# Optimization experiments

Hardware: AMD Instinct MI355X
Metric: run time of the kernel (lower is better)

The kernel has to match this reference:

```python
import jax, jax.numpy as jnp
import numpy as np

EMBED_DIM = 768
NUM_HEADS = 12
HEAD_DIM = EMBED_DIM // NUM_HEADS
SCALE = HEAD_DIM ** -0.5
LN_EPS = 1e-5


def layer_norm(x, gamma, beta):
    mu = jnp.mean(x, axis=-1, keepdims=True)
    var = jnp.var(x, axis=-1, keepdims=True)
    return (x - mu) * jax.lax.rsqrt(var + LN_EPS) * gamma + beta


def setup_inputs() -> dict:
    key = jax.random.key(0)
    ks = jax.random.split(key, 10)
    B, N, M, C = 4, 4096, 256, EMBED_DIM
    inp = {
        "input_tokens": jax.random.normal(ks[0], (B, N, C), dtype=jnp.float32),
        "query_tokens": jax.random.normal(ks[1], (B, M, C), dtype=jnp.float32),
        "Wq": jax.random.normal(ks[2], (C, C), dtype=jnp.float32) * 0.02,
        "bq": jnp.zeros((C,), dtype=jnp.float32),
        "Wk": jax.random.normal(ks[3], (C, C), dtype=jnp.float32) * 0.02,
        "bk": jnp.zeros((C,), dtype=jnp.float32),
        "Wv": jax.random.normal(ks[4], (C, C), dtype=jnp.float32) * 0.02,
        "bv": jnp.zeros((C,), dtype=jnp.float32),
        "gq_ln": jnp.ones((C,), dtype=jnp.float32),
        "bq_ln": jnp.zeros((C,), dtype=jnp.float32),
        "gk_ln": jnp.ones((C,), dtype=jnp.float32),
        "bk_ln": jnp.zeros((C,), dtype=jnp.float32),
    }
    return inp


def reference(input_tokens, query_tokens, Wq, bq, Wk, bk, Wv, bv,
              gq_ln, bq_ln, gk_ln, bk_ln):
    B, N, C = input_tokens.shape
    _, M, _ = query_tokens.shape
    H, D = NUM_HEADS, HEAD_DIM

    # v: Linear only (no LayerNorm on the attn=None path)
    v = (input_tokens @ Wv.T + bv).reshape(B, N, H, D).transpose(0, 2, 1, 3)   # [B,H,N,D]
    # q, k: Linear -> LayerNorm over full embed_dim, then split heads
    q = layer_norm(query_tokens @ Wq.T + bq, gq_ln, bq_ln)
    q = q.reshape(B, M, H, D).transpose(0, 2, 1, 3) * SCALE                    # [B,H,M,D]
    k = layer_norm(input_tokens @ Wk.T + bk, gk_ln, bk_ln)
    k = k.reshape(B, N, H, D).transpose(0, 2, 1, 3)                            # [B,H,N,D]

    attn = jax.nn.softmax(jnp.einsum('bhmd,bhnd->bhmn', q, k), axis=-1)        # [B,H,M,N]
    out = jnp.einsum('bhmn,bhnd->bhmd', attn, v)                               # [B,H,M,D]
    out = out.transpose(0, 2, 1, 3).reshape(B, M, C)
    return (query_tokens + out, attn)
```

## Files before the change

### kernel.cpp

```cpp
#include <hip/hip_runtime.h>
#include <math.h>

#define BB 4
#define NN 4096
#define MM 256
#define CC 768
#define HH 12
#define DD 64
#define SCALEF 0.125f
#define LN_EPSF 1e-5f

typedef __attribute__((ext_vector_type(4))) float f32x4;
typedef __attribute__((ext_vector_type(16))) float f32x16;
typedef __attribute__((ext_vector_type(8))) _Float16 f16x8;
typedef __attribute__((ext_vector_type(4))) _Float16 f16x4;

__device__ __forceinline__ void gldh(const _Float16* g, _Float16* l) {
    __builtin_amdgcn_global_load_lds(
        (const __attribute__((address_space(1))) void*)g,
        (__attribute__((address_space(3))) void*)l, 16, 0, 0);
}

__global__ __launch_bounds__(256) void conv_f16(
    const float* __restrict__ x, _Float16* __restrict__ y, long long n)
{
    long long i = ((long long)blockIdx.x * 256 + threadIdx.x) * 8;
    const long long stride = (long long)gridDim.x * 256 * 8;
    for (; i < n; i += stride) {
        float4 a = *(const float4*)(x + i);
        float4 b = *(const float4*)(x + i + 4);
        f16x8 o;
        o[0] = (_Float16)a.x; o[1] = (_Float16)a.y;
        o[2] = (_Float16)a.z; o[3] = (_Float16)a.w;
        o[4] = (_Float16)b.x; o[5] = (_Float16)b.y;
        o[6] = (_Float16)b.z; o[7] = (_Float16)b.w;
        *(f16x8*)(y + i) = o;
    }
}

__global__ __launch_bounds__(256) void proj_kv_f16(
    const _Float16* __restrict__ Xh,
    const _Float16* __restrict__ X2h,
    const _Float16* __restrict__ Wkh, const _Float16* __restrict__ Wqh,
    const _Float16* __restrict__ Wvh,
    const float* __restrict__ bk, const float* __restrict__ bq,
    const float* __restrict__ bv,
    _Float16* __restrict__ Klin, _Float16* __restrict__ Qlin,
    _Float16* __restrict__ Vth)
{
    __shared__ _Float16 As[2][4096];
    __shared__ _Float16 Bks[2][4096];
    __shared__ _Float16 Bvs[2][4096];

    const int bid = blockIdx.x;
    const _Float16* Ag; const _Float16* Bkg;
    const float* biask; _Float16* outk;
    bool hasV;
    int bm, bn;
    if (bid < 768) {
        bm = bid & 127; bn = bid >> 7;
        Ag = Xh; Bkg = Wkh; biask = bk; outk = Klin; hasV = true;
    } else {
        const int sid = bid - 768;
        bm = sid & 7; bn = sid >> 3;
        Ag = X2h; Bkg = Wqh; biask = bq; outk = Qlin; hasV = false;
    }
    const int row0 = bm * 128, col0 = bn * 128;

    const int tid = threadIdx.x;
    const int w = tid >> 6, lane = tid & 63;
    const int wr = w >> 1, wc = w & 1;
    const int fr = lane & 15, kg = lane >> 4;

    f32x4 acck[4][4], accv[4][4];
#pragma unroll
    for (int m = 0; m < 4; ++m)
#pragma unroll
        for (int n = 0; n < 4; ++n) {
            acck[m][n] = (f32x4){0.f, 0.f, 0.f, 0.f};
            accv[m][n] = (f32x4){0.f, 0.f, 0.f, 0.f};
        }

#define STAGE(sel, kt)                                                           \
    do {                                                                         \
        const int kk = (kt) << 5;                                                \
        _Pragma("unroll")                                                        \
        for (int i = 0; i < 2; ++i) {                                            \
            const int cbase = (i * 4 + w) * 64;                                  \
            const int c = cbase + lane;                                          \
            const int row = c >> 2, ks = (c & 3) << 3;                           \
            gldh(Ag  + (size_t)(row0 + row) * CC + kk + ks, &As[sel][cbase * 8]);\
            gldh(Bkg + (size_t)(col0 + row) * CC + kk + ks, &Bks[sel][cbase * 8]);\
            gldh(Wvh + (size_t)(col0 + row) * CC + kk + ks, &Bvs[sel][cbase * 8]);\
        }                                                                        \
    } while (0)

    STAGE(0, 0);
    int cur = 0;
    const int nk = CC >> 5;
    for (int kt = 0; kt < nk; ++kt) {
        __syncthreads();
        if (kt + 1 < nk) STAGE(cur ^ 1, kt + 1);
        const _Float16* lA = As[cur];
        const _Float16* lBk = Bks[cur];
        const _Float16* lBv = Bvs[cur];
        f16x8 a[4];
#pragma unroll
        for (int m = 0; m < 4; ++m)
            a[m] = *(const f16x8*)(lA + (wr * 64 + m * 16 + fr) * 32 + kg * 8);
#pragma unroll
        for (int n = 0; n < 4; ++n) {
            f16x8 bkf = *(const f16x8*)(lBk + (wc * 64 + n * 16 + fr) * 32 + kg * 8);
            __builtin_amdgcn_s_setprio(1);
#pragma unroll
            for (int m = 0; m < 4; ++m)
                acck[m][n] = __builtin_amdgcn_mfma_f32_16x16x32_f16(
                    a[m], bkf, acck[m][n], 0, 0, 0);
            __builtin_amdgcn_s_setprio(0);
            f16x8 bvf = *(const f16x8*)(lBv + (wc * 64 + n * 16 + fr) * 32 + kg * 8);
            __builtin_amdgcn_s_setprio(1);
#pragma unroll
            for (int m = 0; m < 4; ++m)
                accv[m][n] = __builtin_amdgcn_mfma_f32_16x16x32_f16(
                    a[m], bvf, accv[m][n], 0, 0, 0);
            __builtin_amdgcn_s_setprio(0);
        }
        cur ^= 1;
    }
#undef STAGE

    {
        float bvv[4];
#pragma unroll
        for (int n = 0; n < 4; ++n)
            bvv[n] = biask[col0 + wc * 64 + n * 16 + fr];
#pragma unroll
        for (int m = 0; m < 4; ++m)
#pragma unroll
            for (int n = 0; n < 4; ++n) {
                const int col = col0 + wc * 64 + n * 16 + fr;
#pragma unroll
                for (int r = 0; r < 4; ++r) {
                    const int row = row0 + wr * 64 + m * 16 + kg * 4 + r;
                    outk[(size_t)row * CC + col] = (_Float16)(acck[m][n][r] + bvv[n]);
                }
            }
    }
    if (hasV) {
        const int b = row0 >> 12;
        const int rb = row0 & 4095;
#pragma unroll
        for (int n = 0; n < 4; ++n) {
            const int cg = col0 + wc * 64 + n * 16 + fr;
            const int hh = cg >> 6, d = cg & 63;
            const float bb = bv[cg];
            _Float16* vrow = Vth + ((size_t)((b * HH + hh) * DD + d)) * NN + rb + wr * 64;
#pragma unroll
            for (int m = 0; m < 4; ++m) {
                f16x4 v4;
#pragma unroll
                for (int r = 0; r < 4; ++r)
                    v4[r] = (_Float16)(accv[m][n][r] + bb);
                *(f16x4*)(vrow + m * 16 + kg * 4) = v4;
            }
        }
    }
}

__global__ __launch_bounds__(256) void ln_rows_f16(
    const _Float16* __restrict__ Y, _Float16* __restrict__ outh,
    const float* __restrict__ g, const float* __restrict__ be, const float scale)
{
    const int row = blockIdx.x;
    const _Float16* y = Y + (size_t)row * CC;
    const int tid = threadIdx.x;
    float x0 = (float)y[tid], x1 = (float)y[tid + 256], x2 = (float)y[tid + 512];
    float s = x0 + x1 + x2;
    float q = x0 * x0 + x1 * x1 + x2 * x2;
#pragma unroll
    for (int o = 32; o >= 1; o >>= 1) {
        s += __shfl_xor(s, o, 64);
        q += __shfl_xor(q, o, 64);
    }
    __shared__ float sh_s[4], sh_q[4];
    const int w = tid >> 6;
    if ((tid & 63) == 0) { sh_s[w] = s; sh_q[w] = q; }
    __syncthreads();
    s = sh_s[0] + sh_s[1] + sh_s[2] + sh_s[3];
    q = sh_q[0] + sh_q[1] + sh_q[2] + sh_q[3];
    const float mu  = s * (1.f / 768.f);
    const float var = q * (1.f / 768.f) - mu * mu;
    const float inv = rsqrtf(var + LN_EPSF);
    _Float16* o = outh + (size_t)row * CC;
    o[tid]       = (_Float16)(((x0 - mu) * inv * g[tid]       + be[tid])       * scale);
    o[tid + 256] = (_Float16)(((x1 - mu) * inv * g[tid + 256] + be[tid + 256]) * scale);
    o[tid + 512] = (_Float16)(((x2 - mu) * inv * g[tid + 512] + be[tid + 512]) * scale);
}

__global__ __launch_bounds__(256, 4) void attn_stats(
    const _Float16* __restrict__ Qh,
    const _Float16* __restrict__ Kh,
    float* __restrict__ stats)
{
    __shared__ __align__(16) unsigned char smem[37888];
    _Float16* Kl = (_Float16*)smem;
    _Float16* Ql = (_Float16*)(smem + 32768);
    float (*red)[32][2] = (float(*)[32][2])(smem + 36864);

    const int tid = threadIdx.x;
    const int w = tid >> 6, lane = tid & 63;
    const int l5 = lane >> 5, lm = lane & 31;
    const int bid = blockIdx.x;
    const int mt = bid / 192;
    const int rem = bid % 192;
    const int bh = rem >> 2, ns = rem & 3;
    const int h = bh % HH, b = bh / HH;
    const int qr0 = mt * 32;
    const int nb = ns * 1024;

#define STAGEK(sel, c0)                                                         \
    _Pragma("unroll")                                                           \
    for (int i = 0; i < 4; ++i) {                                               \
        const int L = i * 256 + tid;                                            \
        const int n = L >> 3, pos = L & 7;                                      \
        gldh(Kh + (size_t)(b * NN + (c0) + n) * CC + h * DD + ((pos ^ (n & 7)) << 3), \
             &Kl[(sel) * 8192 + (i * 256 + w * 64) * 8]);                       \
    }

    {
        const int n = tid >> 3, pos = tid & 7;
        gldh(Qh + (size_t)(b * MM + qr0 + n) * CC + h * DD + ((pos ^ (n & 7)) << 3),
             &Ql[(w * 64) * 8]);
    }
    STAGEK(0, nb);
    __syncthreads();
    f16x8 qf[4];
#pragma unroll
    for (int ks = 0; ks < 4; ++ks)
        qf[ks] = *(const f16x8*)&Ql[lm * 64 + (((ks * 2 + l5) ^ (lm & 7)) << 3)];

    const int nl = w * 32 + lm;

    float mrun = -1e30f, srun = 0.f;
    int cur = 0;
    for (int c = 0; c < 8; ++c) {
        if (c) __syncthreads();
        if (c + 1 < 8) STAGEK(cur ^ 1, nb + (c + 1) * 128);
        const _Float16* Kb = Kl + cur * 8192;
        f32x16 s;
#pragma unroll
        for (int r = 0; r < 16; ++r) s[r] = 0.f;
        __builtin_amdgcn_s_setprio(1);
#pragma unroll
        for (int ks = 0; ks < 4; ++ks) {
            f16x8 kf = *(const f16x8*)&Kb[nl * 64 + (((ks * 2 + l5) ^ (nl & 7)) << 3)];
            s = __builtin_amdgcn_mfma_f32_32x32x16_f16(kf, qf[ks], s, 0, 0, 0);
        }
        __builtin_amdgcn_s_setprio(0);
        float cmax = s[0];
#pragma unroll
        for (int r = 1; r < 16; ++r) cmax = fmaxf(cmax, s[r]);
        cmax = fmaxf(cmax, __shfl_xor(cmax, 32, 64));
        const float nm = fmaxf(mrun, cmax);
        float cs = 0.f;
#pragma unroll
        for (int r = 0; r < 16; ++r) cs += __expf(s[r] - nm);
        cs += __shfl_xor(cs, 32, 64);
        srun = srun * __expf(mrun - nm) + cs;
        mrun = nm;
        cur ^= 1;
    }
    if (lane < 32) { red[w][lane][0] = mrun; red[w][lane][1] = srun; }
    __syncthreads();
    if (w == 0 && lane < 32) {
        float M = -1e30f;
#pragma unroll
        for (int ww = 0; ww < 4; ++ww) M = fmaxf(M, red[ww][lane][0]);
        float S = 0.f;
#pragma unroll
        for (int ww = 0; ww < 4; ++ww) S += red[ww][lane][1] * __expf(red[ww][lane][0] - M);
        float* sp = stats + ((size_t)((bh * 8 + mt) * 32 + lane)) * 8 + ns * 2;
        sp[0] = M; sp[1] = S;
    }
#undef STAGEK
}

__global__ __launch_bounds__(256, 2) void attn_main(
    const _Float16* __restrict__ Qh, const _Float16* __restrict__ Kh,
    const _Float16* __restrict__ Vt,
    const float* __restrict__ stats, const float* __restrict__ qtok,
    float* __restrict__ attn, float* __restrict__ out0)
{
    __shared__ __align__(16) unsigned char smem[77824];
    _Float16* Kl = (_Float16*)smem;
    _Float16* Vl = (_Float16*)(smem + 32768);
    _Float16* Ql = (_Float16*)(smem + 65536);
    _Float16* Pl = (_Float16*)(smem + 69632);
    float* rbuf = (float*)smem;

    const int tid = threadIdx.x;
    const int w = tid >> 6, lane = tid & 63;
    const int l5 = lane >> 5, lm = lane & 31;
    const int bh = blockIdx.x % 48;
    const int mt = blockIdx.x / 48;
    const int h = bh % HH, b = bh / HH;
    const int qr0 = mt * 32;

#define STAGEK(sel, c0)                                                         \
    _Pragma("unroll")                                                           \
    for (int i = 0; i < 4; ++i) {                                               \
        const int L = i * 256 + tid;                                            \
        const int n = L >> 3, pos = L & 7;                                      \
        gldh(Kh + (size_t)(b * NN + (c0) + n) * CC + h * DD + ((pos ^ (n & 7)) << 3), \
             &Kl[(sel) * 8192 + (i * 256 + w * 64) * 8]);                       \
    }
#define STAGEV(sel, c0)                                                         \
    _Pragma("unroll")                                                           \
    for (int i = 0; i < 4; ++i) {                                               \
        const int L = i * 256 + tid;                                            \
        const int d = L >> 4, pos = L & 15;                                     \
        const int blk = (pos & 8) | ((pos & 7) ^ (d & 7));                      \
        gldh(Vt + (size_t)(bh * DD + d) * NN + (c0) + blk * 8,                  \
             &Vl[(sel) * 8192 + (i * 256 + w * 64) * 8]);                       \
    }

    float M, invS;
    {
        const float* sp = stats + ((size_t)((bh * 8 + mt) * 32 + lm)) * 8;
        M = -1e30f;
#pragma unroll
        for (int n2 = 0; n2 < 4; ++n2) M = fmaxf(M, sp[n2 * 2]);
        float S = 0.f;
#pragma unroll
        for (int n2 = 0; n2 < 4; ++n2) S += sp[n2 * 2 + 1] * __expf(sp[n2 * 2] - M);
        invS = 1.f / S;
    }

    {
        const int n = tid >> 3, pos = tid & 7;
        gldh(Qh + (size_t)(b * MM + qr0 + n) * CC + h * DD + ((pos ^ (n & 7)) << 3),
             &Ql[(w * 64) * 8]);
    }
    STAGEK(0, 0); STAGEV(0, 0);
    __syncthreads();
    f16x8 qf[4];
#pragma unroll
    for (int ks = 0; ks < 4; ++ks)
        qf[ks] = *(const f16x8*)&Ql[lm * 64 + (((ks * 2 + l5) ^ (lm & 7)) << 3)];

    const int nl = w * 32 + lm;

    f32x16 oacc[2];
#pragma unroll
    for (int dt = 0; dt < 2; ++dt)
#pragma unroll
        for (int r = 0; r < 16; ++r) oacc[dt][r] = 0.f;

    float* attnRow = attn + ((size_t)(bh * MM + qr0 + lm)) * NN;

    int cur = 0;
    for (int c = 0; c < 32; ++c) {
        if (c) __syncthreads();
        if (c + 1 < 32) { STAGEK(cur ^ 1, (c + 1) * 128); STAGEV(cur ^ 1, (c + 1) * 128); }
        const _Float16* Kb = Kl + cur * 8192;
        const _Float16* Vb = Vl + cur * 8192;
        f32x16 s;
#pragma unroll
        for (int r = 0; r < 16; ++r) s[r] = 0.f;
        __builtin_amdgcn_s_setprio(1);
#pragma unroll
        for (int ks = 0; ks < 4; ++ks) {
            f16x8 kf = *(const f16x8*)&Kb[nl * 64 + (((ks * 2 + l5) ^ (nl & 7)) << 3)];
            s = __builtin_amdgcn_mfma_f32_32x32x16_f16(kf, qf[ks], s, 0, 0, 0);
        }
        __builtin_amdgcn_s_setprio(0);
#pragma unroll
        for (int q = 0; q < 4; ++q) {
            float4 pw;
            f16x4 ph;
#pragma unroll
            for (int r = 0; r < 4; ++r) {
                const float p = __expf(s[q * 4 + r] - M) * invS;
                ((float*)&pw)[r] = p;
                ph[r] = (_Float16)p;
            }
            *(float4*)(attnRow + c * 128 + w * 32 + q * 8 + l5 * 4) = pw;
            const int blk16 = w * 4 + q;
            const int pos = (blk16 & 8) | ((blk16 & 7) ^ (lm & 7));
            *(f16x4*)&Pl[lm * 128 + pos * 8 + l5 * 4] = ph;
        }
        __builtin_amdgcn_s_setprio(1);
#pragma unroll
        for (int ks = 0; ks < 2; ++ks) {
            const int blk16 = w * 4 + ks * 2 + l5;
            const int posP = (blk16 & 8) | ((blk16 & 7) ^ (lm & 7));
            f16x8 pf = *(const f16x8*)&Pl[lm * 128 + posP * 8];
#pragma unroll
            for (int dt = 0; dt < 2; ++dt) {
                const int d = dt * 32 + lm;
                const int posV = (blk16 & 8) | ((blk16 & 7) ^ (d & 7));
                f16x8 vf = *(const f16x8*)&Vb[d * 128 + posV * 8];
                oacc[dt] = __builtin_amdgcn_mfma_f32_32x32x16_f16(pf, vf, oacc[dt], 0, 0, 0);
            }
        }
        __builtin_amdgcn_s_setprio(0);
        cur ^= 1;
    }

    __syncthreads();
#pragma unroll
    for (int dt = 0; dt < 2; ++dt)
#pragma unroll
        for (int r = 0; r < 16; ++r) {
            const int mrow = (r & 3) + 8 * (r >> 2) + 4 * l5;
            rbuf[w * 2048 + mrow * 64 + dt * 32 + lm] = oacc[dt][r];
        }
    __syncthreads();
    {
        const int m = tid >> 3, d0 = (tid & 7) * 8;
        const size_t obase = (size_t)(b * MM + qr0 + m) * CC + h * DD + d0;
#pragma unroll
        for (int j = 0; j < 8; ++j) {
            const int idx = m * 64 + d0 + j;
            float v = rbuf[idx] + rbuf[2048 + idx] + rbuf[4096 + idx] + rbuf[6144 + idx];
            out0[obase + j] = v + qtok[obase + j];
        }
    }
#undef STAGEK
#undef STAGEV
}

extern "C" void kernel_launch(void* const* d_in, const int* in_sizes, int n_in,
                              void* d_out, int out_size, void* d_ws, size_t ws_size,
                              hipStream_t stream) {
    (void)in_sizes; (void)n_in; (void)out_size; (void)ws_size;
    const float* input_tokens = (const float*)d_in[0];
    const float* query_tokens = (const float*)d_in[1];
    const float* Wq   = (const float*)d_in[2];
    const float* bq   = (const float*)d_in[3];
    const float* Wk   = (const float*)d_in[4];
    const float* bk   = (const float*)d_in[5];
    const float* Wv   = (const float*)d_in[6];
    const float* bv   = (const float*)d_in[7];
    const float* gq   = (const float*)d_in[8];
    const float* bqln = (const float*)d_in[9];
    const float* gk   = (const float*)d_in[10];
    const float* bkln = (const float*)d_in[11];

    float* out0 = (float*)d_out;
    float* attn = out0 + (size_t)BB * MM * CC;

    _Float16* hptr = (_Float16*)d_ws;
    _Float16* Klin = hptr;
    _Float16* Qlin = Klin + (size_t)BB * NN * CC;
    _Float16* Xh   = Qlin + (size_t)BB * MM * CC;
    _Float16* X2h  = Xh   + (size_t)BB * NN * CC;
    _Float16* Wkh  = X2h  + (size_t)BB * MM * CC;
    _Float16* Wqh  = Wkh  + (size_t)CC * CC;
    _Float16* Wvh  = Wqh  + (size_t)CC * CC;
    _Float16* Kh   = Wvh  + (size_t)CC * CC;
    _Float16* Qh   = Kh   + (size_t)BB * NN * CC;
    _Float16* Vt   = Qh   + (size_t)BB * MM * CC;
    float* stats   = (float*)(Vt + (size_t)BB * HH * DD * NN);

    conv_f16<<<2048, 256, 0, stream>>>(input_tokens, Xh, (long long)BB * NN * CC);
    conv_f16<<<384, 256, 0, stream>>>(query_tokens, X2h, (long long)BB * MM * CC);
    conv_f16<<<288, 256, 0, stream>>>(Wk, Wkh, (long long)CC * CC);
    conv_f16<<<288, 256, 0, stream>>>(Wq, Wqh, (long long)CC * CC);
    conv_f16<<<288, 256, 0, stream>>>(Wv, Wvh, (long long)CC * CC);

    proj_kv_f16<<<816, 256, 0, stream>>>(Xh, X2h, Wkh, Wqh, Wvh,
                                         bk, bq, bv, Klin, Qlin, Vt);

    ln_rows_f16<<<BB * NN, 256, 0, stream>>>(Klin, Kh, gk, bkln, 1.0f);
    ln_rows_f16<<<BB * MM, 256, 0, stream>>>(Qlin, Qh, gq, bqln, SCALEF);

    attn_stats<<<1536, 256, 0, stream>>>(Qh, Kh, stats);
    attn_main<<<384, 256, 0, stream>>>(Qh, Kh, Vt, stats, query_tokens, attn, out0);
}
```

Before: 208.5 us.

## Split attn_main over head-dim halves to double grid size

Splits the attention main kernel's output head dimension into two halves, one per block, doubling the grid from 384 to 768 blocks so more of the GPU's compute units are occupied. Each block now stages only half of V and uses half the LDS, but both blocks recompute the full QK^T scores and exp. Only the dh==0 block writes the attn probability matrix. The output epilogue is vectorized to float4 loads and stores. The cost is duplicated QK and softmax work and duplicated K loads.

After: 238.3 us. +14.3%, slower.

```diff
diff --git a/kernel.cpp b/kernel.cpp
--- a/kernel.cpp
+++ b/kernel.cpp
@@ -291,18 +291,19 @@
     const float* __restrict__ stats, const float* __restrict__ qtok,
     float* __restrict__ attn, float* __restrict__ out0)
 {
-    __shared__ __align__(16) unsigned char smem[77824];
+    __shared__ __align__(16) unsigned char smem[61440];
     _Float16* Kl = (_Float16*)smem;
     _Float16* Vl = (_Float16*)(smem + 32768);
-    _Float16* Ql = (_Float16*)(smem + 65536);
-    _Float16* Pl = (_Float16*)(smem + 69632);
+    _Float16* Ql = (_Float16*)(smem + 49152);
+    _Float16* Pl = (_Float16*)(smem + 53248);
     float* rbuf = (float*)smem;
 
     const int tid = threadIdx.x;
     const int w = tid >> 6, lane = tid & 63;
     const int l5 = lane >> 5, lm = lane & 31;
     const int bh = blockIdx.x % 48;
-    const int mt = blockIdx.x / 48;
+    const int t  = blockIdx.x / 48;
+    const int mt = t >> 1, dh = t & 1;
     const int h = bh % HH, b = bh / HH;
     const int qr0 = mt * 32;
 
@@ -316,12 +317,12 @@
     }
 #define STAGEV(sel, c0)                                                         \
     _Pragma("unroll")                                                           \
-    for (int i = 0; i < 4; ++i) {                                               \
+    for (int i = 0; i < 2; ++i) {                                               \
         const int L = i * 256 + tid;                                            \
         const int d = L >> 4, pos = L & 15;                                     \
         const int blk = (pos & 8) | ((pos & 7) ^ (d & 7));                      \
-        gldh(Vt + (size_t)(bh * DD + d) * NN + (c0) + blk * 8,                  \
-             &Vl[(sel) * 8192 + (i * 256 + w * 64) * 8]);                       \
+        gldh(Vt + (size_t)(bh * DD + dh * 32 + d) * NN + (c0) + blk * 8,        \
+             &Vl[(sel) * 4096 + (i * 256 + w * 64) * 8]);                       \
     }
 
     float M, invS;
@@ -350,11 +351,9 @@
 
     const int nl = w * 32 + lm;
 
-    f32x16 oacc[2];
-#pragma unroll
-    for (int dt = 0; dt < 2; ++dt)
-#pragma unroll
-        for (int r = 0; r < 16; ++r) oacc[dt][r] = 0.f;
+    f32x16 oacc;
+#pragma unroll
+    for (int r = 0; r < 16; ++r) oacc[r] = 0.f;
 
     float* attnRow = attn + ((size_t)(bh * MM + qr0 + lm)) * NN;
 
@@ -363,7 +362,7 @@
         if (c) __syncthreads();
         if (c + 1 < 32) { STAGEK(cur ^ 1, (c + 1) * 128); STAGEV(cur ^ 1, (c + 1) * 128); }
         const _Float16* Kb = Kl + cur * 8192;
-        const _Float16* Vb = Vl + cur * 8192;
+        const _Float16* Vb = Vl + cur * 4096;
         f32x16 s;
 #pragma unroll
         for (int r = 0; r < 16; ++r) s[r] = 0.f;
@@ -384,7 +383,8 @@
                 ((float*)&pw)[r] = p;
                 ph[r] = (_Float16)p;
             }
-            *(float4*)(attnRow + c * 128 + w * 32 + q * 8 + l5 * 4) = pw;
+            if (dh == 0)
+                *(float4*)(attnRow + c * 128 + w * 32 + q * 8 + l5 * 4) = pw;
             const int blk16 = w * 4 + q;
             const int pos = (blk16 & 8) | ((blk16 & 7) ^ (lm & 7));
             *(f16x4*)&Pl[lm * 128 + pos * 8 + l5 * 4] = ph;
@@ -395,13 +395,9 @@
             const int blk16 = w * 4 + ks * 2 + l5;
             const int posP = (blk16 & 8) | ((blk16 & 7) ^ (lm & 7));
             f16x8 pf = *(const f16x8*)&Pl[lm * 128 + posP * 8];
-#pragma unroll
-            for (int dt = 0; dt < 2; ++dt) {
-                const int d = dt * 32 + lm;
-                const int posV = (blk16 & 8) | ((blk16 & 7) ^ (d & 7));
-                f16x8 vf = *(const f16x8*)&Vb[d * 128 + posV * 8];
-                oacc[dt] = __builtin_amdgcn_mfma_f32_32x32x16_f16(pf, vf, oacc[dt], 0, 0, 0);
-            }
+            const int posV = (blk16 & 8) | ((blk16 & 7) ^ (lm & 7));
+            f16x8 vf = *(const f16x8*)&Vb[lm * 128 + posV * 8];
+            oacc = __builtin_amdgcn_mfma_f32_32x32x16_f16(pf, vf, oacc, 0, 0, 0);
         }
         __builtin_amdgcn_s_setprio(0);
         cur ^= 1;
@@ -409,22 +405,23 @@
 
     __syncthreads();
 #pragma unroll
-    for (int dt = 0; dt < 2; ++dt)
-#pragma unroll
-        for (int r = 0; r < 16; ++r) {
-            const int mrow = (r & 3) + 8 * (r >> 2) + 4 * l5;
-            rbuf[w * 2048 + mrow * 64 + dt * 32 + lm] = oacc[dt][r];
-        }
+    for (int r = 0; r < 16; ++r) {
+        const int mrow = (r & 3) + 8 * (r >> 2) + 4 * l5;
+        rbuf[w * 1024 + mrow * 32 + lm] = oacc[r];
+    }
     __syncthreads();
     {
-        const int m = tid >> 3, d0 = (tid & 7) * 8;
-        const size_t obase = (size_t)(b * MM + qr0 + m) * CC + h * DD + d0;
-#pragma unroll
-        for (int j = 0; j < 8; ++j) {
-            const int idx = m * 64 + d0 + j;
-            float v = rbuf[idx] + rbuf[2048 + idx] + rbuf[4096 + idx] + rbuf[6144 + idx];
-            out0[obase + j] = v + qtok[obase + j];
-        }
+        const int m = tid >> 3, d0 = (tid & 7) * 4;
+        const size_t obase = (size_t)(b * MM + qr0 + m) * CC + h * DD + dh * 32 + d0;
+        float4 v;
+#pragma unroll
+        for (int j = 0; j < 4; ++j) {
+            const int idx = m * 32 + d0 + j;
+            ((float*)&v)[j] = rbuf[idx] + rbuf[1024 + idx] + rbuf[2048 + idx] + rbuf[3072 + idx];
+        }
+        float4 q4 = *(const float4*)(qtok + obase);
+        v.x += q4.x; v.y += q4.y; v.z += q4.z; v.w += q4.w;
+        *(float4*)(out0 + obase) = v;
     }
 #undef STAGEK
 #undef STAGEV
@@ -476,5 +473,5 @@
     ln_rows_f16<<<BB * MM, 256, 0, stream>>>(Qlin, Qh, gq, bqln, SCALEF);
 
     attn_stats<<<1536, 256, 0, stream>>>(Qh, Kh, stats);
-    attn_main<<<384, 256, 0, stream>>>(Qh, Kh, Vt, stats, query_tokens, attn, out0);
-}
+    attn_main<<<768, 256, 0, stream>>>(Qh, Kh, Vt, stats, query_tokens, attn, out0);
+}
```
